# Optimization experiments

Hardware: AMD Instinct MI355X
Metric: run time of the kernel (lower is better)

The kernel has to match this reference:

```python
import jax, jax.numpy as jnp
import numpy as np

EMBED_DIM = 4096
MAX_POS = 8192
BASE = 10000.0
B, S = 2, 4096


def _make_freqs_cis(max_positions, embed_dim, base):
    # position * exp(-log(base) * (2i/dim)) -> angle theta_{p,i}
    pos = jnp.arange(max_positions, dtype=jnp.float32)[:, None]          # (P, 1)
    div = jnp.exp(jnp.arange(0, embed_dim, 2, dtype=jnp.float32) * (-np.log(base) / embed_dim))  # (D/2,)
    freqs = pos * div[None, :]                                           # (P, D/2)
    return jnp.stack([jnp.cos(freqs), jnp.sin(freqs)], axis=-1)          # (P, D/2, 2)


def setup_inputs() -> dict:
    key = jax.random.key(0)
    k1, k2 = jax.random.split(key)
    xq = jax.random.normal(k1, (B, S, EMBED_DIM), dtype=jnp.float32)
    xk = jax.random.normal(k2, (B, S, EMBED_DIM), dtype=jnp.float32)
    freqs_cis = _make_freqs_cis(MAX_POS, EMBED_DIM, BASE)
    return {"xq": xq, "xk": xk, "freqs_cis": freqs_cis, "start": 0}


def _rotate(x, cos, sin):
    # x: (B, S, D); cos/sin: (S, D/2) broadcast over batch
    b, s, d = x.shape
    xp = x.reshape(b, s, d // 2, 2)
    even, odd = xp[..., 0], xp[..., 1]
    out_even = even * cos - odd * sin
    out_odd = even * sin + odd * cos
    return jnp.stack([out_even, out_odd], axis=-1).reshape(b, s, d)


def reference(xq, xk, freqs_cis, start):
    seq_len = xq.shape[1]
    fc = freqs_cis[start:start + seq_len]        # (S, D/2, 2)
    cos = fc[:, :, 0][None]                      # (1, S, D/2)
    sin = fc[:, :, 1][None]
    return _rotate(xq, cos, sin), _rotate(xk, cos, sin)
```

## Files before the change

### kernel.cpp

```cpp
#include <hip/hip_runtime.h>


#define S_LEN 4096
#define ROW4  1024

__global__ __launch_bounds__(256) void rope_kernel(
    const float4* __restrict__ xq,
    const float4* __restrict__ xk,
    const float4* __restrict__ freqs,
    const int*    __restrict__ start_p,
    float4* __restrict__ outq,
    float4* __restrict__ outk,
    long long n4)
{
    long long i = (long long)blockIdx.x * blockDim.x + threadIdx.x;
    if (i >= n4) return;

    int row  = (int)(i >> 10);
    int col4 = (int)(i & (ROW4 - 1));
    int s    = row & (S_LEN - 1);
    int pos  = *start_p + s;

    float4 fc = freqs[(long long)pos * ROW4 + col4];
    float4 q  = xq[i];
    float4 k  = xk[i];

    float4 oq, ok;
    oq.x = q.x * fc.x - q.y * fc.y;
    oq.y = q.x * fc.y + q.y * fc.x;
    oq.z = q.z * fc.z - q.w * fc.w;
    oq.w = q.z * fc.w + q.w * fc.z;

    ok.x = k.x * fc.x - k.y * fc.y;
    ok.y = k.x * fc.y + k.y * fc.x;
    ok.z = k.z * fc.z - k.w * fc.w;
    ok.w = k.z * fc.w + k.w * fc.z;

    outq[i] = oq;
    outk[i] = ok;
}

extern "C" void kernel_launch(void* const* d_in, const int* in_sizes, int n_in,
                              void* d_out, int out_size, void* d_ws, size_t ws_size,
                              hipStream_t stream) {
    const float4* xq    = (const float4*)d_in[0];
    const float4* xk    = (const float4*)d_in[1];
    const float4* fc    = (const float4*)d_in[2];
    const int*    start = (const int*)d_in[3];

    long long n  = (long long)in_sizes[0];
    long long n4 = n / 4;

    float4* outq = (float4*)d_out;
    float4* outk = (float4*)((float*)d_out + n);

    int block = 256;
    long long grid = (n4 + block - 1) / block;

    rope_kernel<<<(dim3)(unsigned)grid, block, 0, stream>>>(
        xq, xk, fc, start, outq, outk, n4);
}
```

Measured before the change: 502.3 us.

## Process both batches per thread sharing one freqs load, use nontemporal loads/stores

Each thread now handles the same sequence position for both batch elements, so the freqs vector is loaded once and reused for two batches, halving freqs traffic. Global loads and stores of xq/xk and the outputs use nontemporal builtins to avoid polluting cache with streaming data. The change hardcodes B=2 through the half-split, and it also doubles per-thread work while halving the grid.

```diff
diff --git a/kernel.cpp b/kernel.cpp
--- a/kernel.cpp
+++ b/kernel.cpp
@@ -1,62 +1,71 @@
 #include <hip/hip_runtime.h>
 
+
+typedef float v4f __attribute__((ext_vector_type(4)));
 
 #define S_LEN 4096
 #define ROW4  1024
 
 __global__ __launch_bounds__(256) void rope_kernel(
-    const float4* __restrict__ xq,
-    const float4* __restrict__ xk,
-    const float4* __restrict__ freqs,
-    const int*    __restrict__ start_p,
-    float4* __restrict__ outq,
-    float4* __restrict__ outk,
-    long long n4)
+    const v4f* __restrict__ xq,
+    const v4f* __restrict__ xk,
+    const v4f* __restrict__ freqs,
+    const int* __restrict__ start_p,
+    v4f* __restrict__ outq,
+    v4f* __restrict__ outk,
+    long long half4)
 {
     long long i = (long long)blockIdx.x * blockDim.x + threadIdx.x;
-    if (i >= n4) return;
+    if (i >= half4) return;
 
-    int row  = (int)(i >> 10);
+    int s    = (int)(i >> 10);
     int col4 = (int)(i & (ROW4 - 1));
-    int s    = row & (S_LEN - 1);
     int pos  = *start_p + s;
 
-    float4 fc = freqs[(long long)pos * ROW4 + col4];
-    float4 q  = xq[i];
-    float4 k  = xk[i];
+    v4f fc = freqs[((long long)pos << 10) | col4];
 
-    float4 oq, ok;
-    oq.x = q.x * fc.x - q.y * fc.y;
-    oq.y = q.x * fc.y + q.y * fc.x;
-    oq.z = q.z * fc.z - q.w * fc.w;
-    oq.w = q.z * fc.w + q.w * fc.z;
+    long long i1 = i + half4;
 
-    ok.x = k.x * fc.x - k.y * fc.y;
-    ok.y = k.x * fc.y + k.y * fc.x;
-    ok.z = k.z * fc.z - k.w * fc.w;
-    ok.w = k.z * fc.w + k.w * fc.z;
+    v4f q0 = __builtin_nontemporal_load(xq + i);
+    v4f k0 = __builtin_nontemporal_load(xk + i);
+    v4f q1 = __builtin_nontemporal_load(xq + i1);
+    v4f k1 = __builtin_nontemporal_load(xk + i1);
 
-    outq[i] = oq;
-    outk[i] = ok;
+    v4f oq0, ok0, oq1, ok1;
+    oq0.x = q0.x * fc.x - q0.y * fc.y;  oq0.y = q0.x * fc.y + q0.y * fc.x;
+    oq0.z = q0.z * fc.z - q0.w * fc.w;  oq0.w = q0.z * fc.w + q0.w * fc.z;
+
+    ok0.x = k0.x * fc.x - k0.y * fc.y;  ok0.y = k0.x * fc.y + k0.y * fc.x;
+    ok0.z = k0.z * fc.z - k0.w * fc.w;  ok0.w = k0.z * fc.w + k0.w * fc.z;
+
+    oq1.x = q1.x * fc.x - q1.y * fc.y;  oq1.y = q1.x * fc.y + q1.y * fc.x;
+    oq1.z = q1.z * fc.z - q1.w * fc.w;  oq1.w = q1.z * fc.w + q1.w * fc.z;
+
+    ok1.x = k1.x * fc.x - k1.y * fc.y;  ok1.y = k1.x * fc.y + k1.y * fc.x;
+    ok1.z = k1.z * fc.z - k1.w * fc.w;  ok1.w = k1.z * fc.w + k1.w * fc.z;
+
+    __builtin_nontemporal_store(oq0, outq + i);
+    __builtin_nontemporal_store(ok0, outk + i);
+    __builtin_nontemporal_store(oq1, outq + i1);
+    __builtin_nontemporal_store(ok1, outk + i1);
 }
 
 extern "C" void kernel_launch(void* const* d_in, const int* in_sizes, int n_in,
                               void* d_out, int out_size, void* d_ws, size_t ws_size,
                               hipStream_t stream) {
-    const float4* xq    = (const float4*)d_in[0];
-    const float4* xk    = (const float4*)d_in[1];
-    const float4* fc    = (const float4*)d_in[2];
-    const int*    start = (const int*)d_in[3];
+    const v4f* xq    = (const v4f*)d_in[0];
+    const v4f* xk    = (const v4f*)d_in[1];
+    const v4f* fc    = (const v4f*)d_in[2];
+    const int* start = (const int*)d_in[3];
 
-    long long n  = (long long)in_sizes[0];
-    long long n4 = n / 4;
+    long long n     = (long long)in_sizes[0];
+    long long half4 = n / 4 / 2;
 
-    float4* outq = (float4*)d_out;
-    float4* outk = (float4*)((float*)d_out + n);
+    v4f* outq = (v4f*)d_out;
+    v4f* outk = (v4f*)((float*)d_out + n);
 
     int block = 256;
-    long long grid = (n4 + block - 1) / block;
+    unsigned grid = (unsigned)((half4 + block - 1) / block);
 
-    rope_kernel<<<(dim3)(unsigned)grid, block, 0, stream>>>(
-        xq, xk, fc, start, outq, outk, n4);
+    rope_kernel<<<grid, block, 0, stream>>>(xq, xk, fc, start, outq, outk, half4);
 }
```

Result: no change. 503.1 us (+0.2%).
